# Optimization experiments

Measured on AMD Instinct MI355X. Metric: run time of the kernel, lower is better.

Reference implementation:

```python
import jax, jax.numpy as jnp
import numpy as np

EMBED = 1024
HEADS = 16
HEAD_DIM = EMBED // HEADS
LN_EPS = 1e-5


def _layer_norm(x, g, b):
    m = jnp.mean(x, axis=-1, keepdims=True)
    v = jnp.mean((x - m) ** 2, axis=-1, keepdims=True)
    return (x - m) / jnp.sqrt(v + LN_EPS) * g + b


def _rope(x):
    # x: (b, H, n, D); standard rotary: freqs repeated (cat(freqs, freqs)), rotate_half
    D = x.shape[-1]
    n = x.shape[2]
    inv_freq = 1.0 / (10000.0 ** (jnp.arange(0, D, 2, dtype=jnp.float32) / D))
    freqs = jnp.arange(n, dtype=jnp.float32)[:, None] * inv_freq[None, :]  # (n, D/2)
    emb = jnp.concatenate([freqs, freqs], axis=-1)  # (n, D)
    cos, sin = jnp.cos(emb), jnp.sin(emb)
    rot = jnp.concatenate([-x[..., D // 2:], x[..., : D // 2]], axis=-1)
    return x * cos + rot * sin


def setup_inputs() -> dict:
    key = jax.random.key(0)
    ks = jax.random.split(key, 8)
    E = EMBED
    s_in = 1.0 / np.sqrt(E)
    return {
        "x": jax.random.normal(ks[0], (2, 2048, E), dtype=jnp.float32),
        "in_proj_w": jax.random.uniform(ks[1], (3 * E, E), jnp.float32, -s_in, s_in),
        "in_proj_b": jnp.zeros((3 * E,), jnp.float32),
        "out_proj_w": jax.random.uniform(ks[2], (E, E), jnp.float32, -s_in, s_in),
        "out_proj_b": jnp.zeros((E,), jnp.float32),
        "geglu_w": jax.random.uniform(ks[3], (2 * E, E), jnp.float32, -s_in, s_in),
        "geglu_b": jnp.zeros((2 * E,), jnp.float32),
        "ln1_g": jnp.ones((E,), jnp.float32),
        "ln1_b": jnp.zeros((E,), jnp.float32),
        "ln2_g": jnp.ones((E,), jnp.float32),
        "ln2_b": jnp.zeros((E,), jnp.float32),
    }


def reference(x, in_proj_w, in_proj_b, out_proj_w, out_proj_b,
              geglu_w, geglu_b, ln1_g, ln1_b, ln2_g, ln2_b):
    b, n, E = x.shape
    H, D = HEADS, HEAD_DIM

    # RoPE applied to raw x (q = k = v = x in the module)
    xh = x.reshape(b, n, H, D).transpose(0, 2, 1, 3)  # (b,H,n,D)
    qr = _rope(xh)
    kr = qr  # q and k are identical pre-projection
    q = qr.transpose(0, 2, 1, 3).reshape(b, n, E)
    k = kr.transpose(0, 2, 1, 3).reshape(b, n, E)
    v = x

    # MultiheadAttention (batch-first semantics): in-proj, per-head SDPA, out-proj
    w_q, w_k, w_v = jnp.split(in_proj_w, 3, axis=0)
    b_q, b_k, b_v = jnp.split(in_proj_b, 3, axis=0)
    qp = (q @ w_q.T + b_q).reshape(b, n, H, D).transpose(0, 2, 1, 3)
    kp = (k @ w_k.T + b_k).reshape(b, n, H, D).transpose(0, 2, 1, 3)
    vp = (v @ w_v.T + b_v).reshape(b, n, H, D).transpose(0, 2, 1, 3)
    scores = jnp.einsum("bhqd,bhkd->bhqk", qp, kp) / jnp.sqrt(jnp.float32(D))
    attn = jax.nn.softmax(scores, axis=-1)
    ctx = jnp.einsum("bhqk,bhkd->bhqd", attn, vp)
    ctx = ctx.transpose(0, 2, 1, 3).reshape(b, n, E)
    attn_out = ctx @ out_proj_w.T + out_proj_b

    # residual + LN1
    h = _layer_norm(x + attn_out, ln1_g, ln1_b)

    # GeGLU: Linear(E -> 2E), chunk, value * gelu(gate) (exact erf gelu like torch)
    proj = h @ geglu_w.T + geglu_b
    val, gate = jnp.split(proj, 2, axis=-1)
    fc_out = val * jax.nn.gelu(gate, approximate=False)

    # residual + LN2
    return _layer_norm(h + fc_out, ln2_g, ln2_b)
```

## Files before the change

kernel.cpp:

```cpp
#include <hip/hip_runtime.h>


typedef __bf16 bf16;
typedef bf16 bf16x8 __attribute__((ext_vector_type(8)));
typedef bf16 bf16x4 __attribute__((ext_vector_type(4)));
typedef float f32x4 __attribute__((ext_vector_type(4)));
typedef float f32x16 __attribute__((ext_vector_type(16)));

#define EMB 1024
#define SEQ 2048
#define NTOK 4096
#define NH 16
#define HD 64

__device__ __forceinline__ f32x4 mfma16(bf16x8 a, bf16x8 b, f32x4 c) {
  return __builtin_amdgcn_mfma_f32_16x16x32_bf16(a, b, c, 0, 0, 0);
}
__device__ __forceinline__ f32x16 mfma32(bf16x8 a, bf16x8 b, f32x16 c) {
  return __builtin_amdgcn_mfma_f32_32x32x16_bf16(a, b, c, 0, 0, 0);
}

__device__ __forceinline__ void gll16(const void* g, void* l) {
  __builtin_amdgcn_global_load_lds(
      (const __attribute__((address_space(1))) void*)g,
      (__attribute__((address_space(3))) void*)l, 16, 0, 0);
}

__device__ __forceinline__ unsigned pk2(float a, float b) {
  union { bf16 h[2]; unsigned u; } t;
  t.h[0] = (bf16)a; t.h[1] = (bf16)b;
  return t.u;
}


__global__ __launch_bounds__(256) void rope_cast(
    const float* __restrict__ x, bf16* __restrict__ xb, bf16* __restrict__ qr) {
  int idx = blockIdx.x * 256 + threadIdx.x;
  int row = idx >> 9;
  int i = idx & 511;
  int h = i >> 5, d2 = i & 31;
  int pos = row & (SEQ - 1);
  int c0 = h * HD + d2;
  size_t base = (size_t)row * EMB;
  float x0 = x[base + c0], x1 = x[base + c0 + 32];
  float invf = exp2f(-(float)d2 * 0.4152410118609203f);
  float ang = (float)pos * invf;
  float sn, cs;
  sincosf(ang, &sn, &cs);
  qr[base + c0] = (bf16)(x0 * cs - x1 * sn);
  qr[base + c0 + 32] = (bf16)(x1 * cs + x0 * sn);
  xb[base + c0] = (bf16)x0;
  xb[base + c0 + 32] = (bf16)x1;
}

__global__ __launch_bounds__(256) void cast_all(
    const float* __restrict__ w0, const float* __restrict__ w1,
    const float* __restrict__ w2, bf16* __restrict__ o0,
    bf16* __restrict__ o1, bf16* __restrict__ o2) {
  int i = (blockIdx.x * 256 + threadIdx.x) * 4;
  const float* s; bf16* d; int off;
  if (i < 3 * 1024 * 1024) { s = w0; d = o0; off = i; }
  else if (i < 4 * 1024 * 1024) { s = w1; d = o1; off = i - 3 * 1024 * 1024; }
  else { s = w2; d = o2; off = i - 4 * 1024 * 1024; }
  float4 f = *(const float4*)(s + off);
  d[off] = (bf16)f.x; d[off + 1] = (bf16)f.y;
  d[off + 2] = (bf16)f.z; d[off + 3] = (bf16)f.w;
}

__global__ __launch_bounds__(256) void gemm_in(
    const bf16* __restrict__ Aq, const bf16* __restrict__ Ax,
    const bf16* __restrict__ W, const float* __restrict__ bias,
    bf16* __restrict__ qb, bf16* __restrict__ kv) {
  __shared__ bf16 As[128 * 32];
  __shared__ bf16 Bs[128 * 32];
  const int tid = threadIdx.x, lane = tid & 63, wave = tid >> 6;
  const int quad = lane >> 4, l16 = lane & 15;
  const int m0 = blockIdx.y * 128, n0 = blockIdx.x * 128;
  const bf16* A = (n0 < 2048) ? Aq : Ax;
  const int K = 1024;
  const int wm = (wave >> 1) * 64, wn = (wave & 1) * 64;
  const int srow = wave * 32 + (lane >> 2);
  const int scol = (lane & 3) * 8;
  f32x4 acc[4][4] = {};
  for (int k0 = 0; k0 < K; k0 += 32) {
    __syncthreads();
    gll16(A + (size_t)(m0 + srow) * K + k0 + scol, As + wave * 1024);
    gll16(A + (size_t)(m0 + srow + 16) * K + k0 + scol, As + wave * 1024 + 512);
    gll16(W + (size_t)(n0 + srow) * K + k0 + scol, Bs + wave * 1024);
    gll16(W + (size_t)(n0 + srow + 16) * K + k0 + scol, Bs + wave * 1024 + 512);
    __syncthreads();
    bf16x8 af[4], bw[4];
#pragma unroll
    for (int t = 0; t < 4; ++t) {
      af[t] = *(const bf16x8*)(As + (wm + t * 16 + l16) * 32 + quad * 8);
      bw[t] = *(const bf16x8*)(Bs + (wn + t * 16 + l16) * 32 + quad * 8);
    }
#pragma unroll
    for (int mt = 0; mt < 4; ++mt)
#pragma unroll
      for (int nt = 0; nt < 4; ++nt)
        acc[mt][nt] = mfma16(af[mt], bw[nt], acc[mt][nt]);
  }
  if (n0 < 1024) {
#pragma unroll
    for (int mt = 0; mt < 4; ++mt)
      for (int nt = 0; nt < 4; ++nt) {
        const int n = n0 + wn + nt * 16 + l16;
        const float bv = bias[n];
#pragma unroll
        for (int r = 0; r < 4; ++r) {
          const int m = m0 + wm + mt * 16 + quad * 4 + r;
          qb[(size_t)m * 1024 + n] = (bf16)((acc[mt][nt][r] + bv) * 0.125f);
        }
      }
  } else if (n0 < 2048) {
#pragma unroll
    for (int mt = 0; mt < 4; ++mt)
      for (int nt = 0; nt < 4; ++nt) {
        const int n = n0 + wn + nt * 16 + l16;
        const float bv = bias[n];
        const int kd = n - 1024, hh = kd >> 6, d = kd & 63;
        const int dc = d >> 3, dl = d & 7;
#pragma unroll
        for (int r = 0; r < 4; ++r) {
          const int m = m0 + wm + mt * 16 + quad * 4 + r;
          const int bb = m >> 11, s = m & 2047;
          const int t = s >> 6, kr = s & 63;
          const size_t base = ((size_t)((bb * 16 + hh) * 32 + t)) * 8192;
          kv[base + kr * 64 + ((dc ^ (kr & 7)) << 3) + dl] =
              (bf16)((acc[mt][nt][r] + bv) * 1.4426950408889634f);
        }
      }
  } else {
#pragma unroll
    for (int mt = 0; mt < 4; ++mt)
      for (int nt = 0; nt < 4; ++nt) {
        const int n = n0 + wn + nt * 16 + l16;
        const float bv = bias[n];
        const int vd = n - 2048, hh = vd >> 6, d = vd & 63;
        const int m = m0 + wm + mt * 16 + quad * 4;
        const int bb = m >> 11, s = m & 2047;
        const int t = s >> 6, kt = s & 63;
        const int g = kt >> 4, w = kt & 15;
        const int c = 2 * g + ((w >> 2) & 1);
        const int slot = (w & 8) ? 4 : 0;
        const size_t base = ((size_t)((bb * 16 + hh) * 32 + t)) * 8192 + 4096;
        bf16x4 pkv;
#pragma unroll
        for (int r = 0; r < 4; ++r) pkv[r] = (bf16)(acc[mt][nt][r] + bv);
        *(bf16x4*)(kv + base + d * 64 + ((c ^ (d & 7)) << 3) + slot) = pkv;
      }
  }
}

__global__ __launch_bounds__(256) void gemm_bt(
    const bf16* __restrict__ A, const bf16* __restrict__ W,
    const float* __restrict__ bias,
    float* __restrict__ outF, bf16* __restrict__ outB,
    int M, int N, int K) {
  __shared__ bf16 As[128 * 32];
  __shared__ bf16 Bs[128 * 32];
  const int tid = threadIdx.x, lane = tid & 63, wave = tid >> 6;
  const int quad = lane >> 4, l16 = lane & 15;
  const int m0 = blockIdx.y * 128, n0 = blockIdx.x * 128;
  const int wm = (wave >> 1) * 64, wn = (wave & 1) * 64;
  const int srow = wave * 32 + (lane >> 2);
  const int scol = (lane & 3) * 8;
  f32x4 acc[4][4] = {};
  for (int k0 = 0; k0 < K; k0 += 32) {
    __syncthreads();
    gll16(A + (size_t)(m0 + srow) * K + k0 + scol, As + wave * 1024);
    gll16(A + (size_t)(m0 + srow + 16) * K + k0 + scol, As + wave * 1024 + 512);
    gll16(W + (size_t)(n0 + srow) * K + k0 + scol, Bs + wave * 1024);
    gll16(W + (size_t)(n0 + srow + 16) * K + k0 + scol, Bs + wave * 1024 + 512);
    __syncthreads();
    bf16x8 af[4], bw[4];
#pragma unroll
    for (int t = 0; t < 4; ++t) {
      af[t] = *(const bf16x8*)(As + (wm + t * 16 + l16) * 32 + quad * 8);
      bw[t] = *(const bf16x8*)(Bs + (wn + t * 16 + l16) * 32 + quad * 8);
    }
#pragma unroll
    for (int mt = 0; mt < 4; ++mt)
#pragma unroll
      for (int nt = 0; nt < 4; ++nt)
        acc[mt][nt] = mfma16(af[mt], bw[nt], acc[mt][nt]);
  }
#pragma unroll
  for (int mt = 0; mt < 4; ++mt)
    for (int nt = 0; nt < 4; ++nt) {
      const int n = n0 + wn + nt * 16 + l16;
      const float bv = bias ? bias[n] : 0.0f;
#pragma unroll
      for (int r = 0; r < 4; ++r) {
        const int m = m0 + wm + mt * 16 + quad * 4 + r;
        const float v = acc[mt][nt][r] + bv;
        if (outF) outF[(size_t)m * N + n] = v;
        if (outB) outB[(size_t)m * N + n] = (bf16)v;
      }
    }
}

__global__ __launch_bounds__(256) void gemm_bt64(
    const bf16* __restrict__ A, const bf16* __restrict__ W,
    const float* __restrict__ bias, float* __restrict__ outF,
    int M, int N, int K) {
  __shared__ bf16 As[128 * 32];
  __shared__ bf16 Bs[64 * 32];
  const int tid = threadIdx.x, lane = tid & 63, wave = tid >> 6;
  const int quad = lane >> 4, l16 = lane & 15;
  const int m0 = blockIdx.y * 128, n0 = blockIdx.x * 64;
  const int wm = (wave >> 1) * 64, wn = (wave & 1) * 32;
  const int srow = wave * 32 + (lane >> 2);
  const int srowB = wave * 16 + (lane >> 2);
  const int scol = (lane & 3) * 8;
  f32x4 acc[4][2] = {};
  for (int k0 = 0; k0 < K; k0 += 32) {
    __syncthreads();
    gll16(A + (size_t)(m0 + srow) * K + k0 + scol, As + wave * 1024);
    gll16(A + (size_t)(m0 + srow + 16) * K + k0 + scol, As + wave * 1024 + 512);
    gll16(W + (size_t)(n0 + srowB) * K + k0 + scol, Bs + wave * 512);
    __syncthreads();
    bf16x8 af[4], bw[2];
#pragma unroll
    for (int t = 0; t < 4; ++t)
      af[t] = *(const bf16x8*)(As + (wm + t * 16 + l16) * 32 + quad * 8);
#pragma unroll
    for (int t = 0; t < 2; ++t)
      bw[t] = *(const bf16x8*)(Bs + (wn + t * 16 + l16) * 32 + quad * 8);
#pragma unroll
    for (int mt = 0; mt < 4; ++mt)
#pragma unroll
      for (int nt = 0; nt < 2; ++nt)
        acc[mt][nt] = mfma16(af[mt], bw[nt], acc[mt][nt]);
  }
#pragma unroll
  for (int mt = 0; mt < 4; ++mt)
    for (int nt = 0; nt < 2; ++nt) {
      const int n = n0 + wn + nt * 16 + l16;
      const float bv = bias[n];
#pragma unroll
      for (int r = 0; r < 4; ++r) {
        const int m = m0 + wm + mt * 16 + quad * 4 + r;
        outF[(size_t)m * N + n] = acc[mt][nt][r] + bv;
      }
    }
}

__global__ __launch_bounds__(512, 4) void attn12(
    const bf16* __restrict__ Q, const bf16* __restrict__ KV,
    bf16* __restrict__ ctx) {
  __shared__ __align__(16) bf16 kvb[2][2][8192];
  const int tid = threadIdx.x, lane = tid & 63, wave = tid >> 6;
  const int grp = wave >> 2, lw = wave & 3;
  const int hi = lane >> 5, l31 = lane & 31, l7 = lane & 7;
  const int bid = blockIdx.x;
  const int hb = (bid & 7) * 4 + ((bid >> 3) & 3);
  const int qt = bid >> 5;
  const int h = hb & 15, b = hb >> 4;

  bf16x8 qf[4];
  {
    const int qrow = qt * 128 + lw * 32 + l31;
    const bf16* qp = Q + (size_t)(b * SEQ + qrow) * 1024 + h * HD + hi * 8;
#pragma unroll
    for (int t = 0; t < 4; ++t) qf[t] = *(const bf16x8*)(qp + t * 16);
  }
  const int soff = lw * 2048 + lane * 8;
  const bf16* kvg = KV + ((size_t)((b * NH + h) * 32 + grp * 16)) * 8192 + soff;
  bf16* myb[2] = {&kvb[grp][0][0], &kvb[grp][1][0]};
#pragma unroll
  for (int i = 0; i < 4; ++i)
    gll16(kvg + i * 512, myb[0] + soff + i * 512);

  f32x16 o0 = {}, o1 = {};
  float lpart = 0.0f;
  const f32x16 zf = {};

  for (int t = 0; t < 16; ++t) {
    __syncthreads();
    if (t + 1 < 16) {
      const bf16* src = kvg + (size_t)(t + 1) * 8192;
      bf16* dst = myb[(t + 1) & 1] + soff;
#pragma unroll
      for (int i = 0; i < 4; ++i) gll16(src + i * 512, dst + i * 512);
    }
    const bf16* ks = myb[t & 1];
    const bf16* vs = ks + 4096;
    f32x16 s0, s1;
    __builtin_amdgcn_s_setprio(1);
    {
      const int swc = (hi ^ l7) * 8;
      bf16x8 k0 = *(const bf16x8*)(ks + l31 * 64 + swc);
      bf16x8 k1 = *(const bf16x8*)(ks + (32 + l31) * 64 + swc);
      s0 = mfma32(k0, qf[0], zf);
      s1 = mfma32(k1, qf[0], zf);
    }
#pragma unroll
    for (int tt = 1; tt < 4; ++tt) {
      const int swc = ((tt * 2 + hi) ^ l7) * 8;
      bf16x8 k0 = *(const bf16x8*)(ks + l31 * 64 + swc);
      bf16x8 k1 = *(const bf16x8*)(ks + (32 + l31) * 64 + swc);
      s0 = mfma32(k0, qf[tt], s0);
      s1 = mfma32(k1, qf[tt], s1);
    }
    __builtin_amdgcn_s_setprio(0);
    unsigned u[16];
#pragma unroll
    for (int g = 0; g < 8; ++g) {
      const int base = (g & 3) * 4;
      float e0, e1, e2, e3;
      if (g < 4) {
        e0 = __builtin_amdgcn_exp2f(s0[base]);
        e1 = __builtin_amdgcn_exp2f(s0[base + 1]);
        e2 = __builtin_amdgcn_exp2f(s0[base + 2]);
        e3 = __builtin_amdgcn_exp2f(s0[base + 3]);
      } else {
        e0 = __builtin_amdgcn_exp2f(s1[base]);
        e1 = __builtin_amdgcn_exp2f(s1[base + 1]);
        e2 = __builtin_amdgcn_exp2f(s1[base + 2]);
        e3 = __builtin_amdgcn_exp2f(s1[base + 3]);
      }
      lpart += (e0 + e1) + (e2 + e3);
      u[g * 2] = pk2(e0, e1);
      u[g * 2 + 1] = pk2(e2, e3);
    }
    __builtin_amdgcn_s_setprio(1);
#pragma unroll
    for (int kk = 0; kk < 4; ++kk) {
      union { unsigned w[4]; bf16x8 v; } fw;
      fw.w[0] = u[4 * kk]; fw.w[1] = u[4 * kk + 1];
      fw.w[2] = u[4 * kk + 2]; fw.w[3] = u[4 * kk + 3];
      const int c16 = (2 * kk + hi) ^ l7;
      bf16x8 v0 = *(const bf16x8*)(vs + l31 * 64 + c16 * 8);
      bf16x8 v1 = *(const bf16x8*)(vs + (32 + l31) * 64 + c16 * 8);
      o0 = mfma32(fw.v, v0, o0);
      o1 = mfma32(fw.v, v1, o1);
    }
    __builtin_amdgcn_s_setprio(0);
  }
  __syncthreads();
  float* fred = (float*)&kvb[0][0][0];
  if (grp == 1) {
    float* p = fred + (size_t)(lw * 64 + lane) * 33;
#pragma unroll
    for (int r = 0; r < 16; ++r) { p[r] = o0[r]; p[16 + r] = o1[r]; }
    p[32] = lpart;
  }
  __syncthreads();
  if (grp == 0) {
    const float* p = fred + (size_t)(lw * 64 + lane) * 33;
    float lt = lpart + p[32];
    lt += __shfl_xor(lt, 32, 64);
    float* Lv = fred + 8448 + lw * 32;
    if (lane < 32) Lv[l31] = 1.0f / lt;
#pragma unroll
    for (int r = 0; r < 16; ++r) {
      const int qloc = (r & 3) + 8 * (r >> 2) + 4 * hi;
      const float inv = Lv[qloc];
      const int qrow = qt * 128 + lw * 32 + qloc;
      bf16* cp = ctx + (size_t)(b * SEQ + qrow) * EMB + h * HD;
      cp[l31] = (bf16)((o0[r] + p[r]) * inv);
      cp[32 + l31] = (bf16)((o1[r] + p[16 + r]) * inv);
    }
  }
}

__global__ __launch_bounds__(256) void ln1_k(
    const float* __restrict__ x, const float* __restrict__ ao,
    const float* __restrict__ g, const float* __restrict__ bta,
    float* __restrict__ hF, bf16* __restrict__ hB) {
  int row = blockIdx.x, tid = threadIdx.x;
  const float* xr = x + (size_t)row * EMB;
  const float* ar = ao + (size_t)row * EMB;
  float v[4], s = 0.0f, s2 = 0.0f;
#pragma unroll
  for (int i = 0; i < 4; ++i) {
    float t = xr[tid + i * 256] + ar[tid + i * 256];
    v[i] = t; s += t; s2 += t * t;
  }
#pragma unroll
  for (int off = 1; off < 64; off <<= 1) {
    s += __shfl_xor(s, off, 64);
    s2 += __shfl_xor(s2, off, 64);
  }
  __shared__ float red[8];
  int wave = tid >> 6, lane = tid & 63;
  if (lane == 0) { red[wave] = s; red[4 + wave] = s2; }
  __syncthreads();
  s = red[0] + red[1] + red[2] + red[3];
  s2 = red[4] + red[5] + red[6] + red[7];
  float mean = s * (1.0f / EMB);
  float var = s2 * (1.0f / EMB) - mean * mean;
  float inv = rsqrtf(var + 1e-5f);
#pragma unroll
  for (int i = 0; i < 4; ++i) {
    int c = tid + i * 256;
    float t = (v[i] - mean) * inv * g[c] + bta[c];
    hF[(size_t)row * EMB + c] = t;
    hB[(size_t)row * EMB + c] = (bf16)t;
  }
}

__global__ __launch_bounds__(256) void geglu_ln2(
    const float* __restrict__ h, const bf16* __restrict__ proj,
    const float* __restrict__ g, const float* __restrict__ bta,
    float* __restrict__ out) {
  int row = blockIdx.x, tid = threadIdx.x;
  const float* hr = h + (size_t)row * EMB;
  const bf16* pr = proj + (size_t)row * 2048;
  float v[4], s = 0.0f, s2 = 0.0f;
#pragma unroll
  for (int i = 0; i < 4; ++i) {
    int c = tid + i * 256;
    float val = (float)pr[c];
    float gate = (float)pr[1024 + c];
    float ge = 0.5f * gate * (1.0f + erff(gate * 0.70710678f));
    float t = hr[c] + val * ge;
    v[i] = t; s += t; s2 += t * t;
  }
#pragma unroll
  for (int off = 1; off < 64; off <<= 1) {
    s += __shfl_xor(s, off, 64);
    s2 += __shfl_xor(s2, off, 64);
  }
  __shared__ float red[8];
  int wave = tid >> 6, lane = tid & 63;
  if (lane == 0) { red[wave] = s; red[4 + wave] = s2; }
  __syncthreads();
  s = red[0] + red[1] + red[2] + red[3];
  s2 = red[4] + red[5] + red[6] + red[7];
  float mean = s * (1.0f / EMB);
  float var = s2 * (1.0f / EMB) - mean * mean;
  float inv = rsqrtf(var + 1e-5f);
#pragma unroll
  for (int i = 0; i < 4; ++i) {
    int c = tid + i * 256;
    out[(size_t)row * EMB + c] = (v[i] - mean) * inv * g[c] + bta[c];
  }
}

extern "C" void kernel_launch(void* const* d_in, const int* in_sizes, int n_in,
                              void* d_out, int out_size, void* d_ws, size_t ws_size,
                              hipStream_t stream) {
  const float* x = (const float*)d_in[0];
  const float* inW = (const float*)d_in[1];
  const float* inB = (const float*)d_in[2];
  const float* outW = (const float*)d_in[3];
  const float* opB = (const float*)d_in[4];
  const float* ggW = (const float*)d_in[5];
  const float* ggB = (const float*)d_in[6];
  const float* g1 = (const float*)d_in[7];
  const float* b1 = (const float*)d_in[8];
  const float* g2 = (const float*)d_in[9];
  const float* b2 = (const float*)d_in[10];
  float* out = (float*)d_out;
  char* ws = (char*)d_ws;
  const size_t MB = 1ull << 20;
  bf16* xb = (bf16*)(ws);
  bf16* hB = (bf16*)(ws);
  bf16* qr = (bf16*)(ws + 8 * MB);
  bf16* ctx = (bf16*)(ws + 8 * MB);
  bf16* wI = (bf16*)(ws + 16 * MB);
  bf16* wO = (bf16*)(ws + 22 * MB);
  bf16* wG = (bf16*)(ws + 24 * MB);
  bf16* qb = (bf16*)(ws + 28 * MB);
  bf16* kv = (bf16*)(ws + 36 * MB);
  bf16* projB = (bf16*)(ws + 28 * MB);
  float* ao = (float*)(ws + 52 * MB);

  rope_cast<<<NTOK * 512 / 256, 256, 0, stream>>>(x, xb, qr);
  cast_all<<<6144, 256, 0, stream>>>(inW, outW, ggW, wI, wO, wG);
  gemm_in<<<dim3(24, 32), 256, 0, stream>>>(qr, xb, wI, inB, qb, kv);
  attn12<<<512, 512, 0, stream>>>(qb, kv, ctx);
  gemm_bt64<<<dim3(16, 32), 256, 0, stream>>>(ctx, wO, opB, ao,
                                              NTOK, 1024, 1024);
  ln1_k<<<NTOK, 256, 0, stream>>>(x, ao, g1, b1, ao, hB);
  gemm_bt<<<dim3(16, 32), 256, 0, stream>>>(hB, wG, ggB, nullptr, projB,
                                            NTOK, 2048, 1024);
  geglu_ln2<<<NTOK, 256, 0, stream>>>(ao, projB, g2, b2, out);
}
```

Baseline: 278.2 us.

## Drop split-KV wave groups in attention, use triple-buffered KV pipeline

The attention kernel previously ran two wave groups per block, each covering half of the KV sequence, then merged partial outputs through shared memory. It now uses 4 waves that each walk all 32 KV tiles, with a three-slot LDS ring buffer, explicit vmcnt waits and raw barriers, so loads run two tiles ahead. This removes the cross-group reduction and halves threads per block, in exchange for a longer serial loop per wave and possibly lower occupancy.

```diff
diff --git a/kernel.cpp b/kernel.cpp
--- a/kernel.cpp
+++ b/kernel.cpp
@@ -247,12 +247,12 @@
     }
 }
 
-__global__ __launch_bounds__(512, 4) void attn12(
+__global__ __launch_bounds__(256, 3) void attn13(
     const bf16* __restrict__ Q, const bf16* __restrict__ KV,
     bf16* __restrict__ ctx) {
-  __shared__ __align__(16) bf16 kvb[2][2][8192];
+  __shared__ __align__(16) bf16 kvb[3][8192];
+  __shared__ float Linv[4][32];
   const int tid = threadIdx.x, lane = tid & 63, wave = tid >> 6;
-  const int grp = wave >> 2, lw = wave & 3;
   const int hi = lane >> 5, l31 = lane & 31, l7 = lane & 7;
   const int bid = blockIdx.x;
   const int hb = (bid & 7) * 4 + ((bid >> 3) & 3);
@@ -261,31 +261,39 @@
 
   bf16x8 qf[4];
   {
-    const int qrow = qt * 128 + lw * 32 + l31;
+    const int qrow = qt * 128 + wave * 32 + l31;
     const bf16* qp = Q + (size_t)(b * SEQ + qrow) * 1024 + h * HD + hi * 8;
 #pragma unroll
     for (int t = 0; t < 4; ++t) qf[t] = *(const bf16x8*)(qp + t * 16);
   }
-  const int soff = lw * 2048 + lane * 8;
-  const bf16* kvg = KV + ((size_t)((b * NH + h) * 32 + grp * 16)) * 8192 + soff;
-  bf16* myb[2] = {&kvb[grp][0][0], &kvb[grp][1][0]};
+  asm volatile("s_waitcnt vmcnt(0)" ::: "memory");
+
+  const int soff = tid * 8;
+  const bf16* kvg = KV + ((size_t)(b * NH + h) * 32) * 8192 + soff;
 #pragma unroll
   for (int i = 0; i < 4; ++i)
-    gll16(kvg + i * 512, myb[0] + soff + i * 512);
+    gll16(kvg + i * 2048, kvb[0] + soff + i * 2048);
+#pragma unroll
+  for (int i = 0; i < 4; ++i)
+    gll16(kvg + 8192 + i * 2048, kvb[1] + soff + i * 2048);
 
   f32x16 o0 = {}, o1 = {};
   float lpart = 0.0f;
   const f32x16 zf = {};
-
-  for (int t = 0; t < 16; ++t) {
-    __syncthreads();
-    if (t + 1 < 16) {
-      const bf16* src = kvg + (size_t)(t + 1) * 8192;
-      bf16* dst = myb[(t + 1) & 1] + soff;
-#pragma unroll
-      for (int i = 0; i < 4; ++i) gll16(src + i * 512, dst + i * 512);
-    }
-    const bf16* ks = myb[t & 1];
+  int rd = 0, wr = 2;
+
+  for (int t = 0; t < 32; ++t) {
+    if (t < 31) asm volatile("s_waitcnt vmcnt(4)" ::: "memory");
+    else        asm volatile("s_waitcnt vmcnt(0)" ::: "memory");
+    __builtin_amdgcn_s_barrier();
+    __builtin_amdgcn_sched_barrier(0);
+    if (t + 2 < 32) {
+      const bf16* src = kvg + (size_t)(t + 2) * 8192;
+      bf16* dst = kvb[wr] + soff;
+#pragma unroll
+      for (int i = 0; i < 4; ++i) gll16(src + i * 2048, dst + i * 2048);
+    }
+    const bf16* ks = kvb[rd];
     const bf16* vs = ks + 4096;
     f32x16 s0, s1;
     __builtin_amdgcn_s_setprio(1);
@@ -338,31 +346,19 @@
       o1 = mfma32(fw.v, v1, o1);
     }
     __builtin_amdgcn_s_setprio(0);
-  }
-  __syncthreads();
-  float* fred = (float*)&kvb[0][0][0];
-  if (grp == 1) {
-    float* p = fred + (size_t)(lw * 64 + lane) * 33;
-#pragma unroll
-    for (int r = 0; r < 16; ++r) { p[r] = o0[r]; p[16 + r] = o1[r]; }
-    p[32] = lpart;
-  }
-  __syncthreads();
-  if (grp == 0) {
-    const float* p = fred + (size_t)(lw * 64 + lane) * 33;
-    float lt = lpart + p[32];
-    lt += __shfl_xor(lt, 32, 64);
-    float* Lv = fred + 8448 + lw * 32;
-    if (lane < 32) Lv[l31] = 1.0f / lt;
-#pragma unroll
-    for (int r = 0; r < 16; ++r) {
-      const int qloc = (r & 3) + 8 * (r >> 2) + 4 * hi;
-      const float inv = Lv[qloc];
-      const int qrow = qt * 128 + lw * 32 + qloc;
-      bf16* cp = ctx + (size_t)(b * SEQ + qrow) * EMB + h * HD;
-      cp[l31] = (bf16)((o0[r] + p[r]) * inv);
-      cp[32 + l31] = (bf16)((o1[r] + p[16 + r]) * inv);
-    }
+    rd = (rd + 1 == 3) ? 0 : rd + 1;
+    wr = (wr + 1 == 3) ? 0 : wr + 1;
+  }
+  float ltot = lpart + __shfl_xor(lpart, 32, 64);
+  if (lane < 32) Linv[wave][lane] = 1.0f / ltot;
+#pragma unroll
+  for (int r = 0; r < 16; ++r) {
+    const int qloc = (r & 3) + 8 * (r >> 2) + 4 * hi;
+    const float inv = Linv[wave][qloc];
+    const int qrow = qt * 128 + wave * 32 + qloc;
+    bf16* cp = ctx + (size_t)(b * SEQ + qrow) * EMB + h * HD;
+    cp[l31] = (bf16)(o0[r] * inv);
+    cp[32 + l31] = (bf16)(o1[r] * inv);
   }
 }
 
@@ -472,7 +468,7 @@
   rope_cast<<<NTOK * 512 / 256, 256, 0, stream>>>(x, xb, qr);
   cast_all<<<6144, 256, 0, stream>>>(inW, outW, ggW, wI, wO, wG);
   gemm_in<<<dim3(24, 32), 256, 0, stream>>>(qr, xb, wI, inB, qb, kv);
-  attn12<<<512, 512, 0, stream>>>(qb, kv, ctx);
+  attn13<<<512, 256, 0, stream>>>(qb, kv, ctx);
   gemm_bt64<<<dim3(16, 32), 256, 0, stream>>>(ctx, wO, opB, ao,
                                               NTOK, 1024, 1024);
   ln1_k<<<NTOK, 256, 0, stream>>>(x, ao, g1, b1, ao, hB);
```

Measured after the change: 276.3 us. About the same (-0.7%).
